# Kernel tuning notes

Measured on AMD Instinct MI355X. Metric: run time of the kernel, lower is better.

The kernel has to match this reference:

```python
import jax, jax.numpy as jnp
import numpy as np


def _conv(x, w, pad):
    # NCHW conv, stride 1
    return jax.lax.conv_general_dilated(
        x, w, window_strides=(1, 1), padding=pad,
        dimension_numbers=("NCHW", "OIHW", "NCHW"))


def _deform_conv(x, off_w, off_b, w, b, kh, kw, ph, pw):
    """DCNv2-style modulated deformable conv, stride 1, zero padding."""
    B, C, H, W = x.shape
    K = kh * kw
    om = _conv(x, off_w, ((ph, ph), (pw, pw))) + off_b[None, :, None, None]  # [B,3K,H,W]
    dy, dx, m = om[:, :K], om[:, K:2 * K], om[:, 2 * K:]
    mask = jax.nn.sigmoid(m)  # [B,K,H,W]
    ky = (jnp.repeat(jnp.arange(kh), kw) - ph).astype(x.dtype)  # [K]
    kx = (jnp.tile(jnp.arange(kw), kh) - pw).astype(x.dtype)    # [K]
    hh = jnp.arange(H, dtype=x.dtype)[None, None, :, None]
    ww = jnp.arange(W, dtype=x.dtype)[None, None, None, :]
    py = dy + ky[None, :, None, None] + hh  # [B,K,H,W] sampling y
    px = dx + kx[None, :, None, None] + ww  # [B,K,H,W] sampling x
    y0 = jnp.floor(py)
    x0 = jnp.floor(px)
    ty = py - y0
    tx = px - x0
    y0i = y0.astype(jnp.int32)
    x0i = x0.astype(jnp.int32)
    bidx = jnp.arange(B)[:, None, None, None]

    def gather(yi, xi):
        valid = (yi >= 0) & (yi < H) & (xi >= 0) & (xi < W)
        yc = jnp.clip(yi, 0, H - 1)
        xc = jnp.clip(xi, 0, W - 1)
        v = x[bidx, :, yc, xc]  # [B,K,H,W,C]
        return v * valid[..., None].astype(x.dtype)

    val = (gather(y0i, x0i) * ((1 - ty) * (1 - tx))[..., None]
           + gather(y0i, x0i + 1) * ((1 - ty) * tx)[..., None]
           + gather(y0i + 1, x0i) * (ty * (1 - tx))[..., None]
           + gather(y0i + 1, x0i + 1) * (ty * tx)[..., None])
    val = val * mask[..., None]  # modulation
    out = jnp.einsum('bkhwc,ock->bohw', val, w.reshape(w.shape[0], C, K))
    return out + b[None, :, None, None]


def _preprocess(x, w1, b1, w2, b2):
    h = _conv(x, w1, ((0, 0), (0, 0))) + b1[None, :, None, None]
    return _conv(h, w2, ((0, 0), (0, 0))) + b2[None, :, None, None]


def setup_inputs() -> dict:
    key = jax.random.key(0)
    ks = jax.random.split(key, 12)
    B, C, H, W = 4, 64, 256, 256
    k = 3
    s = 0.05
    inp = {
        "a_low": jax.random.normal(ks[0], (B, C, H, W), jnp.float32),
        "a_high": jax.random.normal(ks[1], (B, C, H, W), jnp.float32),
        # preprocess: Conv 64->32 (1x1), Conv 32->64 (1x1)
        "pre_w1": jax.random.normal(ks[2], (C // 2, C, 1, 1), jnp.float32) * s,
        "pre_b1": jnp.zeros((C // 2,), jnp.float32),
        "pre_w2": jax.random.normal(ks[3], (C, C // 2, 1, 1), jnp.float32) * s,
        "pre_b2": jnp.zeros((C,), jnp.float32),
        # column DCN (3x1 kernel): offset/mask conv -> 3*K channels, K=3
        "offc_w": jax.random.normal(ks[4], (3 * k, C, k, 1), jnp.float32) * 0.01,
        "offc_b": jnp.zeros((3 * k,), jnp.float32),
        "wc": jax.random.normal(ks[5], (C, C, k, 1), jnp.float32) * s,
        "bc": jnp.zeros((C,), jnp.float32),
        # row DCN (1x3 kernel)
        "offr_w": jax.random.normal(ks[6], (3 * k, C, 1, k), jnp.float32) * 0.01,
        "offr_b": jnp.zeros((3 * k,), jnp.float32),
        "wr": jax.random.normal(ks[7], (C, C, 1, k), jnp.float32) * s,
        "br": jnp.zeros((C,), jnp.float32),
    }
    return inp


def reference(a_low, a_high, pre_w1, pre_b1, pre_w2, pre_b2,
              offc_w, offc_b, wc, bc, offr_w, offr_b, wr, br):
    a_low = _preprocess(a_low, pre_w1, pre_b1, pre_w2, pre_b2)
    a_high = _preprocess(a_high, pre_w1, pre_b1, pre_w2, pre_b2)
    # column DCN: kernel (3,1), padding (1,0)
    a_low_c = _deform_conv(a_low, offc_w, offc_b, wc, bc, 3, 1, 1, 0)
    a_colum = a_low + jax.nn.sigmoid(a_low_c) * a_high
    # row DCN: kernel (1,3), padding (0,1)
    a_low_r = _deform_conv(a_low, offr_w, offr_b, wr, br, 1, 3, 0, 1)
    a_row = a_low + jax.nn.sigmoid(a_low_r) * a_high
    return a_row + a_colum
```

## Files before the change

kernel.cpp:

```cpp
#include <hip/hip_runtime.h>
#include <hip/hip_fp16.h>
#include <cmath>

namespace {
constexpr int Bn = 4, Cn = 64, Hn = 256, Wn = 256;
constexpr int HWn = Hn * Wn;
constexpr size_t OFF_PRE_LOW  = 0;
constexpr size_t OFF_PRE_HIGH = 33554432;
constexpr size_t OFF_OM_COL   = 67108864;
constexpr size_t OFF_OM_ROW   = 76546048;
constexpr size_t OFF_WOF16    = 85999616;
constexpr size_t OFF_WPACK    = 86013440;
constexpr size_t OFF_WPRE     = 86062592;
constexpr size_t OFF_BEFF     = 86070784;

constexpr int L_WIN  = 0;
constexpr int L_MOFF = 25920;
constexpr int L_MW   = 27456;
constexpr int L_CRD  = 28992;
constexpr int L_MSK  = 29760;
constexpr int L_ZL   = 30528;
constexpr int L_TOT  = 30672;
}

typedef _Float16 f16x8 __attribute__((ext_vector_type(8)));
typedef float f32x4 __attribute__((ext_vector_type(4)));

__device__ __forceinline__ float sigm(float x) { return 1.f / (1.f + __expf(-x)); }
__device__ __forceinline__ __half2 bc2(unsigned u) { return __builtin_bit_cast(__half2, u); }
__device__ __forceinline__ unsigned u32of(__half2 h) { return __builtin_bit_cast(unsigned, h); }

__global__ void k_repack(const float* __restrict__ pw1, const float* __restrict__ pw2,
                         const float* __restrict__ b1,  const float* __restrict__ b2,
                         const float* __restrict__ owc, const float* __restrict__ owr,
                         const float* __restrict__ wc,  const float* __restrict__ wr,
                         char* __restrict__ ws8)
{
    unsigned* Wo2  = (unsigned*)(ws8 + OFF_WOF16);
    __half*   Wp   = (__half*)(ws8 + OFF_WPACK);
    __half*   Wpre = (__half*)(ws8 + OFF_WPRE);
    float*    Beff = (float*)(ws8 + OFF_BEFF);
    int t = blockIdx.x * 256 + threadIdx.x;
    int stride = gridDim.x * 256;
    for (int i = t; i < 3456; i += stride) {
        int ck = i / 18, d = i - ck * 18;
        float v = (d < 9) ? owc[d * 192 + ck] : owr[(d - 9) * 192 + ck];
        Wo2[i] = u32of(__float2half2_rn(v));
    }
    for (int i = t; i < 24576; i += stride) {
        int m = i >= 12288;
        int rem = i - m * 12288;
        int e = rem & 7, l = (rem >> 3) & 63, os = (rem >> 9) & 3, s = rem >> 11;
        int kk = 32 * s + (l >> 4) * 8 + e;
        int o = os * 16 + (l & 15);
        int c = kk & 63, tap = kk >> 6;
        const float* src = m ? wr : wc;
        Wp[i] = __float2half(src[o * 192 + c * 3 + tap]);
    }
    for (int i = t; i < 4096; i += stride) {
        int e = i & 7, l = (i >> 3) & 63, os = (i >> 9) & 3, s = i >> 11;
        int o = os * 16 + (l & 15);
        int c = 32 * s + (l >> 4) * 8 + e;
        float a = 0.f;
        for (int j = 0; j < 32; j++) a += pw2[o * 32 + j] * pw1[j * 64 + c];
        Wpre[i] = __float2half(a);
    }
    for (int i = t; i < 64; i += stride) {
        float a = b2[i];
        for (int j = 0; j < 32; j++) a += pw2[i * 32 + j] * b1[j];
        Beff[i] = a;
    }
}

__global__ __launch_bounds__(256) void k_pre(const float* __restrict__ alow,
                                             const float* __restrict__ ahigh,
                                             char* __restrict__ ws8,
                                             __half* __restrict__ anchw)
{
    __shared__ __align__(16) char XSb[32768];
    int bid = blockIdx.x;
    int tensor = bid >> 10;
    int r = bid & 1023;
    int b = r >> 8, h = r & 255;
    const float* __restrict__ x = (tensor ? ahigh : alow)
                                  + (size_t)b * Cn * HWn + (size_t)h * Wn;
    int tid = threadIdx.x;

#pragma unroll
    for (int it = 0; it < 4; it++) {
        int job = tid + it * 256;
        int c4 = job >> 6, pxg = job & 63;
        int c0 = c4 * 4;
        float4 f0 = *reinterpret_cast<const float4*>(x + (size_t)(c0 + 0) * HWn + pxg * 4);
        float4 f1 = *reinterpret_cast<const float4*>(x + (size_t)(c0 + 1) * HWn + pxg * 4);
        float4 f2 = *reinterpret_cast<const float4*>(x + (size_t)(c0 + 2) * HWn + pxg * 4);
        float4 f3 = *reinterpret_cast<const float4*>(x + (size_t)(c0 + 3) * HWn + pxg * 4);
        const float* p0 = reinterpret_cast<const float*>(&f0);
        const float* p1 = reinterpret_cast<const float*>(&f1);
        const float* p2 = reinterpret_cast<const float*>(&f2);
        const float* p3 = reinterpret_cast<const float*>(&f3);
        int u = c4 >> 1, hf = c4 & 1;
#pragma unroll
        for (int i = 0; i < 4; i++) {
            int px = pxg * 4 + i;
            uint2 v;
            v.x = u32of(__float22half2_rn({p0[i], p1[i]}));
            v.y = u32of(__float22half2_rn({p2[i], p3[i]}));
            *reinterpret_cast<uint2*>(XSb + px * 128 + ((u ^ (px & 7)) * 16) + hf * 8) = v;
        }
    }
    __syncthreads();

    int wv = tid >> 6, lane = tid & 63;
    int kq = lane >> 4, n = lane & 15;
    const f16x8* __restrict__ Wf = (const f16x8*)(ws8 + OFF_WPRE);
    const float* __restrict__ beff = (const float*)(ws8 + OFF_BEFF);
    f16x8 af[8];
#pragma unroll
    for (int i = 0; i < 8; i++) af[i] = Wf[i * 64 + lane];
    f32x4 zero = {0.f, 0.f, 0.f, 0.f};
    f32x4 acc[16];
#pragma unroll
    for (int i = 0; i < 16; i++) acc[i] = zero;
#pragma unroll
    for (int s = 0; s < 2; s++) {
#pragma unroll
        for (int pt = 0; pt < 4; pt++) {
            int px = wv * 64 + pt * 16 + n;
            int u = (4 * s + kq) ^ (px & 7);
            f16x8 bf = *reinterpret_cast<const f16x8*>(XSb + px * 128 + u * 16);
#pragma unroll
            for (int os = 0; os < 4; os++)
                acc[os * 4 + pt] = __builtin_amdgcn_mfma_f32_16x16x32_f16(
                    af[s * 4 + os], bf, acc[os * 4 + pt], 0, 0, 0);
        }
    }
#pragma unroll
    for (int os = 0; os < 4; os++) {
        float4 bq = *reinterpret_cast<const float4*>(beff + os * 16 + kq * 4);
        const float* bqp = reinterpret_cast<const float*>(&bq);
#pragma unroll
        for (int pt = 0; pt < 4; pt++)
#pragma unroll
            for (int rg = 0; rg < 4; rg++) acc[os * 4 + pt][rg] += bqp[rg];
    }

    {
        __half* __restrict__ outp = (__half*)(ws8 + (tensor ? OFF_PRE_HIGH : OFF_PRE_LOW))
                                    + (size_t)r * 16384;
#pragma unroll
        for (int os = 0; os < 4; os++)
#pragma unroll
            for (int pt = 0; pt < 4; pt++) {
                int px = wv * 64 + pt * 16 + n;
                uint2 v;
                v.x = u32of(__float22half2_rn({acc[os * 4 + pt][0], acc[os * 4 + pt][1]}));
                v.y = u32of(__float22half2_rn({acc[os * 4 + pt][2], acc[os * 4 + pt][3]}));
                *reinterpret_cast<uint2*>(outp + (size_t)px * 64 + os * 16 + kq * 4) = v;
            }
    }
    if (tensor == 0) {
        __half* __restrict__ np = anchw + (size_t)b * Cn * HWn + (size_t)h * Wn;
#pragma unroll
        for (int os = 0; os < 4; os++)
#pragma unroll
            for (int rg = 0; rg < 4; rg++) {
                int o = os * 16 + kq * 4 + rg;
#pragma unroll
                for (int pt = 0; pt < 4; pt++) {
                    int px = wv * 64 + pt * 16 + n;
                    np[(size_t)o * HWn + px] = __float2half(acc[os * 4 + pt][rg]);
                }
            }
    }
}

__global__ __launch_bounds__(256) void k_om2(const __half* __restrict__ Anc,
                                             const float* __restrict__ ocb,
                                             const float* __restrict__ orb,
                                             char* __restrict__ ws8)
{
    const unsigned* __restrict__ Wo2 = (const unsigned*)(ws8 + OFF_WOF16);
    int blk = blockIdx.x;
    int h = blk & 255, b = blk >> 8;
    int tid = threadIdx.x;
    int q2 = tid & 127, md = tid >> 7;
    int w0 = q2 * 2;
    const __half* __restrict__ base = Anc + ((size_t)b * Cn) * HWn + (size_t)h * Wn + w0;

    const bool topOK = (h > 0), botOK = (h < Hn - 1);
    const bool lOK = (w0 > 0), rOK = (w0 + 2 < Wn);
    const int offT = topOK ? -Wn : 0;
    const int offB = botOK ? Wn : 0;
    const int offL = lOK ? -1 : 0;
    const int offR = rOK ? 2 : 1;

    const __half2 z = __float2half2_rn(0.f);
    const __half hz = __float2half(0.f);
    __half2 a[9];
#pragma unroll
    for (int d = 0; d < 9; d++) a[d] = z;

    if (md == 0) {
        for (int c = 0; c < 64; c++) {
            const __half* pc = base + (size_t)c * HWn;
            unsigned qm = *reinterpret_cast<const unsigned*>(pc + offT);
            unsigned q0 = *reinterpret_cast<const unsigned*>(pc);
            unsigned qp = *reinterpret_cast<const unsigned*>(pc + offB);
            __half2 m0 = topOK ? bc2(qm) : z;
            __half2 c0 = bc2(q0);
            __half2 p0 = botOK ? bc2(qp) : z;
            const unsigned* wb = Wo2 + c * 54;
#pragma unroll
            for (int d = 0; d < 9; d++) {
                __half2 u0 = bc2(wb[d]), u1 = bc2(wb[18 + d]), u2 = bc2(wb[36 + d]);
                a[d] = __hfma2(u0, m0, __hfma2(u1, c0, __hfma2(u2, p0, a[d])));
            }
        }
        float* __restrict__ omc = (float*)(ws8 + OFF_OM_COL);
        size_t ob = ((size_t)b * 9) * HWn + (size_t)h * Wn + w0;
#pragma unroll
        for (int d = 0; d < 9; d++) {
            float bcd = ocb[d];
            float2 vc = { __low2float(a[d]) + bcd, __high2float(a[d]) + bcd };
            *reinterpret_cast<float2*>(omc + ob + (size_t)d * HWn) = vc;
        }
    } else {
        for (int c = 0; c < 64; c++) {
            const __half* pc = base + (size_t)c * HWn;
            unsigned q0 = *reinterpret_cast<const unsigned*>(pc);
            __half L = lOK ? pc[offL] : hz;
            __half R = rOK ? pc[offR] : hz;
            __half2 c0 = bc2(q0);
            __half2 X = __halves2half2(L, __low2half(c0));
            __half2 Z = __halves2half2(__high2half(c0), R);
            const unsigned* wb = Wo2 + c * 54;
#pragma unroll
            for (int d = 0; d < 9; d++) {
                __half2 v0 = bc2(wb[9 + d]), v1 = bc2(wb[27 + d]), v2 = bc2(wb[45 + d]);
                a[d] = __hfma2(v0, X, __hfma2(v1, c0, __hfma2(v2, Z, a[d])));
            }
        }
        float* __restrict__ omr = (float*)(ws8 + OFF_OM_ROW);
        size_t ob = ((size_t)b * 9) * HWn + (size_t)h * Wn + w0;
#pragma unroll
        for (int d = 0; d < 9; d++) {
            float brd = orb[d];
            float2 vr = { __low2float(a[d]) + brd, __high2float(a[d]) + brd };
            *reinterpret_cast<float2*>(omr + ob + (size_t)d * HWn) = vr;
        }
    }
}

__global__ __launch_bounds__(256, 5) void k_dfuse(const float* __restrict__ bc,
                                                  const float* __restrict__ br,
                                                  float* __restrict__ out,
                                                  char* __restrict__ ws8)
{
    __shared__ __align__(16) char smem8[L_TOT];

    const __half* __restrict__ A16 = (const __half*)(ws8 + OFF_PRE_LOW);

    int bid = blockIdx.x;
    int blk = (bid & 7) * 1024 + (bid >> 3);
    int wt = blk & 7, bh = blk >> 3, h = bh & 255, b = bh >> 8;
    int w0 = wt * 32;
    int tid = threadIdx.x;
    int pbase = b * HWn;

    {
        int ylo = h - 2, xlo = w0 - 2;
#pragma unroll
        for (int i = 0; i < 6; i++) {
            int idx = tid + i * 256;
            if (idx < 1440) {
                int pixw = idx >> 3, ch = idx & 7;
                int r = pixw / 36;
                int xi = pixw - r * 36;
                int y = min(max(ylo + r, 0), Hn - 1);
                int x = min(max(xlo + xi, 0), Wn - 1);
                size_t src = ((size_t)pbase + y * Wn + x) * 64 + ch * 8;
                *reinterpret_cast<uint4*>(smem8 + L_WIN + pixw * 144 + ch * 16) =
                    *reinterpret_cast<const uint4*>(A16 + src);
            }
        }
    }
    if (tid >= 192 && tid < 201) {
        uint4 z4 = {0u, 0u, 0u, 0u};
        *reinterpret_cast<uint4*>(smem8 + L_ZL + (tid - 192) * 16) = z4;
    }

    if (tid < 192) {
        int m = tid >= 96 ? 1 : 0;
        int jj = tid - m * 96;
        int p = jj & 31, tap = jj >> 5;
        int w = w0 + p;
        const float* __restrict__ om = (const float*)(ws8 + (m ? OFF_OM_ROW : OFF_OM_COL));
        size_t ob = ((size_t)b * 9 * Hn + h) * Wn + w;
        float dy = om[ob + (size_t)tap * HWn];
        float dx = om[ob + (size_t)(3 + tap) * HWn];
        float mm = om[ob + (size_t)(6 + tap) * HWn];
        float mask = sigm(mm);
        float py = dy + (float)h + (m ? 0.f : (float)(tap - 1));
        float px = dx + (float)w + (m ? (float)(tap - 1) : 0.f);
        float fy = floorf(py), fx = floorf(px);
        float ty = py - fy, tx = px - fx;
        int y0 = (int)fy, x0 = (int)fx;
        int y1 = y0 + 1, x1 = x0 + 1;
        float vy0 = ((unsigned)y0 < (unsigned)Hn) ? 1.f : 0.f;
        float vy1 = ((unsigned)y1 < (unsigned)Hn) ? 1.f : 0.f;
        float vx0 = ((unsigned)x0 < (unsigned)Wn) ? 1.f : 0.f;
        float vx1 = ((unsigned)x1 < (unsigned)Wn) ? 1.f : 0.f;
        int y0c = min(max(y0, 0), Hn - 1), y1c = min(max(y1, 0), Hn - 1);
        int x0c = min(max(x0, 0), Wn - 1), x1c = min(max(x1, 0), Wn - 1);
        float ry = 1.f - ty, rx = 1.f - tx;
        float w00 = ry * rx * mask * vy0 * vx0;
        float w01 = ry * tx * mask * vy0 * vx1;
        float w10 = ty * rx * mask * vy1 * vx0;
        float w11 = ty * tx * mask * vy1 * vx1;
        int yw0 = y0c - (h - 2), yw1 = y1c - (h - 2);
        int xw0 = x0c - (w0 - 2), xw1 = x1c - (w0 - 2);
        bool i00 = ((unsigned)yw0 < 5u) && ((unsigned)xw0 < 36u);
        bool i01 = ((unsigned)yw0 < 5u) && ((unsigned)xw1 < 36u);
        bool i10 = ((unsigned)yw1 < 5u) && ((unsigned)xw0 < 36u);
        bool i11 = ((unsigned)yw1 < 5u) && ((unsigned)xw1 < 36u);
        ushort4 offs;
        offs.x = i00 ? (ushort)((yw0 * 36 + xw0) * 144) : (ushort)L_ZL;
        offs.y = i01 ? (ushort)((yw0 * 36 + xw1) * 144) : (ushort)L_ZL;
        offs.z = i10 ? (ushort)((yw1 * 36 + xw0) * 144) : (ushort)L_ZL;
        offs.w = i11 ? (ushort)((yw1 * 36 + xw1) * 144) : (ushort)L_ZL;
        *reinterpret_cast<ushort4*>(smem8 + L_MOFF + tid * 8) = offs;
        __half* mw = reinterpret_cast<__half*>(smem8 + L_MW + tid * 8);
        mw[0] = __float2half(w00); mw[1] = __float2half(w01);
        mw[2] = __float2half(w10); mw[3] = __float2half(w11);
        uchar4 cr = { (unsigned char)y0c, (unsigned char)x0c,
                      (unsigned char)y1c, (unsigned char)x1c };
        *reinterpret_cast<uchar4*>(smem8 + L_CRD + tid * 4) = cr;
        unsigned msk = (i00 ? 0u : 1u) | (i01 ? 0u : 2u) | (i10 ? 0u : 4u) | (i11 ? 0u : 8u);
        *reinterpret_cast<unsigned*>(smem8 + L_MSK + tid * 4) = msk;
    }
    __syncthreads();

    int wv = tid >> 6, lane = tid & 63;
    int m = wv >> 1, pg = wv & 1;
    int n = lane & 15, kq = lane >> 4;
    int p = pg * 16 + n;
    const f16x8* __restrict__ Wf = (const f16x8*)(ws8 + OFF_WPACK + (size_t)m * 24576);

    f32x4 zero = {0.f, 0.f, 0.f, 0.f};
    f32x4 acc[4] = {zero, zero, zero, zero};
    ushort4 offs = {0, 0, 0, 0};
    __half2 wh0 = {}, wh1 = {}, wh2 = {}, wh3 = {};
    unsigned msk = 0;
    uchar4 cr = {0, 0, 0, 0};
#pragma unroll
    for (int s = 0; s < 6; s++) {
        if ((s & 1) == 0) {
            int idx = m * 96 + (s >> 1) * 32 + p;
            offs = *reinterpret_cast<const ushort4*>(smem8 + L_MOFF + idx * 8);
            uint2 wr_ = *reinterpret_cast<const uint2*>(smem8 + L_MW + idx * 8);
            __half2 wa = bc2(wr_.x), wb = bc2(wr_.y);
            wh0 = __half2half2(__low2half(wa));
            wh1 = __half2half2(__high2half(wa));
            wh2 = __half2half2(__low2half(wb));
            wh3 = __half2half2(__high2half(wb));
            msk = *reinterpret_cast<const unsigned*>(smem8 + L_MSK + idx * 4);
            cr = *reinterpret_cast<const uchar4*>(smem8 + L_CRD + idx * 4);
        }
        int co = ((s & 1) << 6) + kq * 16;
        uint4 u0 = *reinterpret_cast<const uint4*>(smem8 + (int)offs.x + co);
        uint4 u1 = *reinterpret_cast<const uint4*>(smem8 + (int)offs.y + co);
        uint4 u2 = *reinterpret_cast<const uint4*>(smem8 + (int)offs.z + co);
        uint4 u3 = *reinterpret_cast<const uint4*>(smem8 + (int)offs.w + co);
        __half2 a0 = __hmul2(bc2(u0.x), wh0);
        __half2 a1 = __hmul2(bc2(u0.y), wh0);
        __half2 a2 = __hmul2(bc2(u0.z), wh0);
        __half2 a3 = __hmul2(bc2(u0.w), wh0);
        a0 = __hfma2(bc2(u1.x), wh1, a0); a1 = __hfma2(bc2(u1.y), wh1, a1);
        a2 = __hfma2(bc2(u1.z), wh1, a2); a3 = __hfma2(bc2(u1.w), wh1, a3);
        a0 = __hfma2(bc2(u2.x), wh2, a0); a1 = __hfma2(bc2(u2.y), wh2, a1);
        a2 = __hfma2(bc2(u2.z), wh2, a2); a3 = __hfma2(bc2(u2.w), wh2, a3);
        a0 = __hfma2(bc2(u3.x), wh3, a0); a1 = __hfma2(bc2(u3.y), wh3, a1);
        a2 = __hfma2(bc2(u3.z), wh3, a2); a3 = __hfma2(bc2(u3.w), wh3, a3);
        if (__any(msk != 0)) {
            int cog = ((s & 1) << 5) + kq * 8;
            if (msk & 1u) {
                int gx = (pbase + (int)cr.x * Wn + (int)cr.y) * 64;
                uint4 u = *reinterpret_cast<const uint4*>(A16 + gx + cog);
                a0 = __hfma2(bc2(u.x), wh0, a0); a1 = __hfma2(bc2(u.y), wh0, a1);
                a2 = __hfma2(bc2(u.z), wh0, a2); a3 = __hfma2(bc2(u.w), wh0, a3); }
            if (msk & 2u) {
                int gx = (pbase + (int)cr.x * Wn + (int)cr.w) * 64;
                uint4 u = *reinterpret_cast<const uint4*>(A16 + gx + cog);
                a0 = __hfma2(bc2(u.x), wh1, a0); a1 = __hfma2(bc2(u.y), wh1, a1);
                a2 = __hfma2(bc2(u.z), wh1, a2); a3 = __hfma2(bc2(u.w), wh1, a3); }
            if (msk & 4u) {
                int gx = (pbase + (int)cr.z * Wn + (int)cr.y) * 64;
                uint4 u = *reinterpret_cast<const uint4*>(A16 + gx + cog);
                a0 = __hfma2(bc2(u.x), wh2, a0); a1 = __hfma2(bc2(u.y), wh2, a1);
                a2 = __hfma2(bc2(u.z), wh2, a2); a3 = __hfma2(bc2(u.w), wh2, a3); }
            if (msk & 8u) {
                int gx = (pbase + (int)cr.z * Wn + (int)cr.w) * 64;
                uint4 u = *reinterpret_cast<const uint4*>(A16 + gx + cog);
                a0 = __hfma2(bc2(u.x), wh3, a0); a1 = __hfma2(bc2(u.y), wh3, a1);
                a2 = __hfma2(bc2(u.z), wh3, a2); a3 = __hfma2(bc2(u.w), wh3, a3); }
        }
        uint4 hb = { u32of(a0), u32of(a1), u32of(a2), u32of(a3) };
        f16x8 bf = __builtin_bit_cast(f16x8, hb);
#pragma unroll
        for (int os = 0; os < 4; os++)
            acc[os] = __builtin_amdgcn_mfma_f32_16x16x32_f16(Wf[(s * 4 + os) * 64 + lane], bf, acc[os], 0, 0, 0);
    }

    const float* __restrict__ bias = m ? br : bc;
    float sg[4][4];
#pragma unroll
    for (int os = 0; os < 4; os++) {
        float4 bq = *reinterpret_cast<const float4*>(bias + os * 16 + kq * 4);
        const float* bqp = reinterpret_cast<const float*>(&bq);
#pragma unroll
        for (int rg = 0; rg < 4; rg++) sg[os][rg] = sigm(acc[os][rg] + bqp[rg]);
    }
    __syncthreads();
    float* EXf = reinterpret_cast<float*>(smem8);
#pragma unroll
    for (int os = 0; os < 4; os++)
#pragma unroll
        for (int rg = 0; rg < 4; rg++)
            EXf[m * 2176 + (os * 16 + kq * 4 + rg) * 34 + p] = sg[os][rg];
    __syncthreads();

    int p2 = tid & 31, og = tid >> 5;
    int o0 = og * 8;
    size_t pix = ((size_t)b * Hn + h) * Wn + (w0 + p2);
    uint4 ua = *reinterpret_cast<const uint4*>(A16 + pix * 64 + o0);
    const __half* ap = reinterpret_cast<const __half*>(&ua);
    const __half* __restrict__ Ah16 = (const __half*)(ws8 + OFF_PRE_HIGH);
    uint4 uh = *reinterpret_cast<const uint4*>(Ah16 + pix * 64 + o0);
    const __half* hp = reinterpret_cast<const __half*>(&uh);
    size_t chbase = ((size_t)b * 64 + o0) * HWn + (size_t)h * Wn + (w0 + p2);
#pragma unroll
    for (int j = 0; j < 8; j++) {
        float sc = EXf[(o0 + j) * 34 + p2];
        float sr = EXf[2176 + (o0 + j) * 34 + p2];
        float av = __half2float(ap[j]);
        float hv = __half2float(hp[j]);
        out[chbase + (size_t)j * HWn] = 2.f * av + (sc + sr) * hv;
    }
}

extern "C" void kernel_launch(void* const* d_in, const int* in_sizes, int n_in,
                              void* d_out, int out_size, void* d_ws, size_t ws_size,
                              hipStream_t stream)
{
    const float* a_low  = (const float*)d_in[0];
    const float* a_high = (const float*)d_in[1];
    const float* pre_w1 = (const float*)d_in[2];
    const float* pre_b1 = (const float*)d_in[3];
    const float* pre_w2 = (const float*)d_in[4];
    const float* pre_b2 = (const float*)d_in[5];
    const float* offc_w = (const float*)d_in[6];
    const float* offc_b = (const float*)d_in[7];
    const float* wc     = (const float*)d_in[8];
    const float* bc     = (const float*)d_in[9];
    const float* offr_w = (const float*)d_in[10];
    const float* offr_b = (const float*)d_in[11];
    const float* wr     = (const float*)d_in[12];
    const float* br     = (const float*)d_in[13];
    float* out = (float*)d_out;
    char* ws8  = (char*)d_ws;

    hipLaunchKernelGGL(k_repack, dim3(128), dim3(256), 0, stream,
                       pre_w1, pre_w2, pre_b1, pre_b2, offc_w, offr_w, wc, wr, ws8);
    hipLaunchKernelGGL(k_pre, dim3(2048), dim3(256), 0, stream,
                       a_low, a_high, ws8, (__half*)d_out);
    hipLaunchKernelGGL(k_om2, dim3(1024), dim3(256), 0, stream,
                       (const __half*)d_out, offc_b, offr_b, ws8);
    hipLaunchKernelGGL(k_dfuse, dim3(8192), dim3(256), 0, stream,
                       bc, br, out, ws8);
}
```

Baseline: 157.9 us.

## Store offset maps in fp16, add block-uniform in-window fast path, vectorize epilogue LDS

The offset/mask conv output is now written and read as fp16 instead of fp32, halving that intermediate traffic. A __syncthreads_or over per-sample out-of-window flags lets blocks where every sample falls inside the shared-memory window skip the global-fallback branch and its mask/coordinate loads. The sampling offsets and weights for all three taps are preloaded into registers up front. The sigmoid exchange buffer is transposed to pixel-major so writes and reads use float4 LDS accesses. The change costs offset precision (fp16 rounding of dy/dx before floor) and adds register pressure from the hoisted tap data.

```diff
diff --git a/kernel.cpp b/kernel.cpp
--- a/kernel.cpp
+++ b/kernel.cpp
@@ -8,7 +8,7 @@
 constexpr size_t OFF_PRE_LOW  = 0;
 constexpr size_t OFF_PRE_HIGH = 33554432;
 constexpr size_t OFF_OM_COL   = 67108864;
-constexpr size_t OFF_OM_ROW   = 76546048;
+constexpr size_t OFF_OM_ROW   = 71827456;
 constexpr size_t OFF_WOF16    = 85999616;
 constexpr size_t OFF_WPACK    = 86013440;
 constexpr size_t OFF_WPRE     = 86062592;
@@ -217,13 +217,12 @@
                 a[d] = __hfma2(u0, m0, __hfma2(u1, c0, __hfma2(u2, p0, a[d])));
             }
         }
-        float* __restrict__ omc = (float*)(ws8 + OFF_OM_COL);
+        __half* __restrict__ omc = (__half*)(ws8 + OFF_OM_COL);
         size_t ob = ((size_t)b * 9) * HWn + (size_t)h * Wn + w0;
 #pragma unroll
         for (int d = 0; d < 9; d++) {
-            float bcd = ocb[d];
-            float2 vc = { __low2float(a[d]) + bcd, __high2float(a[d]) + bcd };
-            *reinterpret_cast<float2*>(omc + ob + (size_t)d * HWn) = vc;
+            __half2 v = __hadd2(a[d], __float2half2_rn(ocb[d]));
+            *reinterpret_cast<unsigned*>(omc + ob + (size_t)d * HWn) = u32of(v);
         }
     } else {
         for (int c = 0; c < 64; c++) {
@@ -241,13 +240,12 @@
                 a[d] = __hfma2(v0, X, __hfma2(v1, c0, __hfma2(v2, Z, a[d])));
             }
         }
-        float* __restrict__ omr = (float*)(ws8 + OFF_OM_ROW);
+        __half* __restrict__ omr = (__half*)(ws8 + OFF_OM_ROW);
         size_t ob = ((size_t)b * 9) * HWn + (size_t)h * Wn + w0;
 #pragma unroll
         for (int d = 0; d < 9; d++) {
-            float brd = orb[d];
-            float2 vr = { __low2float(a[d]) + brd, __high2float(a[d]) + brd };
-            *reinterpret_cast<float2*>(omr + ob + (size_t)d * HWn) = vr;
+            __half2 v = __hadd2(a[d], __float2half2_rn(orb[d]));
+            *reinterpret_cast<unsigned*>(omr + ob + (size_t)d * HWn) = u32of(v);
         }
     }
 }
@@ -290,16 +288,17 @@
         *reinterpret_cast<uint4*>(smem8 + L_ZL + (tid - 192) * 16) = z4;
     }
 
+    int myMsk = 0;
     if (tid < 192) {
         int m = tid >= 96 ? 1 : 0;
         int jj = tid - m * 96;
         int p = jj & 31, tap = jj >> 5;
         int w = w0 + p;
-        const float* __restrict__ om = (const float*)(ws8 + (m ? OFF_OM_ROW : OFF_OM_COL));
+        const __half* __restrict__ om = (const __half*)(ws8 + (m ? OFF_OM_ROW : OFF_OM_COL));
         size_t ob = ((size_t)b * 9 * Hn + h) * Wn + w;
-        float dy = om[ob + (size_t)tap * HWn];
-        float dx = om[ob + (size_t)(3 + tap) * HWn];
-        float mm = om[ob + (size_t)(6 + tap) * HWn];
+        float dy = __half2float(om[ob + (size_t)tap * HWn]);
+        float dx = __half2float(om[ob + (size_t)(3 + tap) * HWn]);
+        float mm = __half2float(om[ob + (size_t)(6 + tap) * HWn]);
         float mask = sigm(mm);
         float py = dy + (float)h + (m ? 0.f : (float)(tap - 1));
         float px = dx + (float)w + (m ? (float)(tap - 1) : 0.f);
@@ -336,10 +335,10 @@
         uchar4 cr = { (unsigned char)y0c, (unsigned char)x0c,
                       (unsigned char)y1c, (unsigned char)x1c };
         *reinterpret_cast<uchar4*>(smem8 + L_CRD + tid * 4) = cr;
-        unsigned msk = (i00 ? 0u : 1u) | (i01 ? 0u : 2u) | (i10 ? 0u : 4u) | (i11 ? 0u : 8u);
-        *reinterpret_cast<unsigned*>(smem8 + L_MSK + tid * 4) = msk;
-    }
-    __syncthreads();
+        myMsk = (i00 ? 0 : 1) | (i01 ? 0 : 2) | (i10 ? 0 : 4) | (i11 ? 0 : 8);
+        *reinterpret_cast<unsigned*>(smem8 + L_MSK + tid * 4) = (unsigned)myMsk;
+    }
+    int anyOOW = __syncthreads_or(myMsk);
 
     int wv = tid >> 6, lane = tid & 63;
     int m = wv >> 1, pg = wv & 1;
@@ -347,70 +346,93 @@
     int p = pg * 16 + n;
     const f16x8* __restrict__ Wf = (const f16x8*)(ws8 + OFF_WPACK + (size_t)m * 24576);
 
+    ushort4 offs[3];
+    __half2 wh[3][4];
+#pragma unroll
+    for (int t3 = 0; t3 < 3; t3++) {
+        int idx = m * 96 + t3 * 32 + p;
+        offs[t3] = *reinterpret_cast<const ushort4*>(smem8 + L_MOFF + idx * 8);
+        uint2 wr_ = *reinterpret_cast<const uint2*>(smem8 + L_MW + idx * 8);
+        __half2 wa = bc2(wr_.x), wb = bc2(wr_.y);
+        wh[t3][0] = __half2half2(__low2half(wa));
+        wh[t3][1] = __half2half2(__high2half(wa));
+        wh[t3][2] = __half2half2(__low2half(wb));
+        wh[t3][3] = __half2half2(__high2half(wb));
+    }
+
     f32x4 zero = {0.f, 0.f, 0.f, 0.f};
     f32x4 acc[4] = {zero, zero, zero, zero};
-    ushort4 offs = {0, 0, 0, 0};
-    __half2 wh0 = {}, wh1 = {}, wh2 = {}, wh3 = {};
-    unsigned msk = 0;
-    uchar4 cr = {0, 0, 0, 0};
-#pragma unroll
-    for (int s = 0; s < 6; s++) {
-        if ((s & 1) == 0) {
-            int idx = m * 96 + (s >> 1) * 32 + p;
-            offs = *reinterpret_cast<const ushort4*>(smem8 + L_MOFF + idx * 8);
-            uint2 wr_ = *reinterpret_cast<const uint2*>(smem8 + L_MW + idx * 8);
-            __half2 wa = bc2(wr_.x), wb = bc2(wr_.y);
-            wh0 = __half2half2(__low2half(wa));
-            wh1 = __half2half2(__high2half(wa));
-            wh2 = __half2half2(__low2half(wb));
-            wh3 = __half2half2(__high2half(wb));
-            msk = *reinterpret_cast<const unsigned*>(smem8 + L_MSK + idx * 4);
-            cr = *reinterpret_cast<const uchar4*>(smem8 + L_CRD + idx * 4);
-        }
-        int co = ((s & 1) << 6) + kq * 16;
-        uint4 u0 = *reinterpret_cast<const uint4*>(smem8 + (int)offs.x + co);
-        uint4 u1 = *reinterpret_cast<const uint4*>(smem8 + (int)offs.y + co);
-        uint4 u2 = *reinterpret_cast<const uint4*>(smem8 + (int)offs.z + co);
-        uint4 u3 = *reinterpret_cast<const uint4*>(smem8 + (int)offs.w + co);
-        __half2 a0 = __hmul2(bc2(u0.x), wh0);
-        __half2 a1 = __hmul2(bc2(u0.y), wh0);
-        __half2 a2 = __hmul2(bc2(u0.z), wh0);
-        __half2 a3 = __hmul2(bc2(u0.w), wh0);
-        a0 = __hfma2(bc2(u1.x), wh1, a0); a1 = __hfma2(bc2(u1.y), wh1, a1);
-        a2 = __hfma2(bc2(u1.z), wh1, a2); a3 = __hfma2(bc2(u1.w), wh1, a3);
-        a0 = __hfma2(bc2(u2.x), wh2, a0); a1 = __hfma2(bc2(u2.y), wh2, a1);
-        a2 = __hfma2(bc2(u2.z), wh2, a2); a3 = __hfma2(bc2(u2.w), wh2, a3);
-        a0 = __hfma2(bc2(u3.x), wh3, a0); a1 = __hfma2(bc2(u3.y), wh3, a1);
-        a2 = __hfma2(bc2(u3.z), wh3, a2); a3 = __hfma2(bc2(u3.w), wh3, a3);
-        if (__any(msk != 0)) {
-            int cog = ((s & 1) << 5) + kq * 8;
-            if (msk & 1u) {
-                int gx = (pbase + (int)cr.x * Wn + (int)cr.y) * 64;
-                uint4 u = *reinterpret_cast<const uint4*>(A16 + gx + cog);
-                a0 = __hfma2(bc2(u.x), wh0, a0); a1 = __hfma2(bc2(u.y), wh0, a1);
-                a2 = __hfma2(bc2(u.z), wh0, a2); a3 = __hfma2(bc2(u.w), wh0, a3); }
-            if (msk & 2u) {
-                int gx = (pbase + (int)cr.x * Wn + (int)cr.w) * 64;
-                uint4 u = *reinterpret_cast<const uint4*>(A16 + gx + cog);
-                a0 = __hfma2(bc2(u.x), wh1, a0); a1 = __hfma2(bc2(u.y), wh1, a1);
-                a2 = __hfma2(bc2(u.z), wh1, a2); a3 = __hfma2(bc2(u.w), wh1, a3); }
-            if (msk & 4u) {
-                int gx = (pbase + (int)cr.z * Wn + (int)cr.y) * 64;
-                uint4 u = *reinterpret_cast<const uint4*>(A16 + gx + cog);
-                a0 = __hfma2(bc2(u.x), wh2, a0); a1 = __hfma2(bc2(u.y), wh2, a1);
-                a2 = __hfma2(bc2(u.z), wh2, a2); a3 = __hfma2(bc2(u.w), wh2, a3); }
-            if (msk & 8u) {
-                int gx = (pbase + (int)cr.z * Wn + (int)cr.w) * 64;
-                uint4 u = *reinterpret_cast<const uint4*>(A16 + gx + cog);
-                a0 = __hfma2(bc2(u.x), wh3, a0); a1 = __hfma2(bc2(u.y), wh3, a1);
-                a2 = __hfma2(bc2(u.z), wh3, a2); a3 = __hfma2(bc2(u.w), wh3, a3); }
-        }
-        uint4 hb = { u32of(a0), u32of(a1), u32of(a2), u32of(a3) };
-        f16x8 bf = __builtin_bit_cast(f16x8, hb);
-#pragma unroll
-        for (int os = 0; os < 4; os++)
-            acc[os] = __builtin_amdgcn_mfma_f32_16x16x32_f16(Wf[(s * 4 + os) * 64 + lane], bf, acc[os], 0, 0, 0);
-    }
+
+#define GBLEND(T, CO, A0, A1, A2, A3)                                            \
+    {                                                                            \
+        uint4 u0 = *reinterpret_cast<const uint4*>(smem8 + (int)offs[T].x + (CO)); \
+        uint4 u1 = *reinterpret_cast<const uint4*>(smem8 + (int)offs[T].y + (CO)); \
+        uint4 u2 = *reinterpret_cast<const uint4*>(smem8 + (int)offs[T].z + (CO)); \
+        uint4 u3 = *reinterpret_cast<const uint4*>(smem8 + (int)offs[T].w + (CO)); \
+        A0 = __hmul2(bc2(u0.x), wh[T][0]); A1 = __hmul2(bc2(u0.y), wh[T][0]);    \
+        A2 = __hmul2(bc2(u0.z), wh[T][0]); A3 = __hmul2(bc2(u0.w), wh[T][0]);    \
+        A0 = __hfma2(bc2(u1.x), wh[T][1], A0); A1 = __hfma2(bc2(u1.y), wh[T][1], A1); \
+        A2 = __hfma2(bc2(u1.z), wh[T][1], A2); A3 = __hfma2(bc2(u1.w), wh[T][1], A3); \
+        A0 = __hfma2(bc2(u2.x), wh[T][2], A0); A1 = __hfma2(bc2(u2.y), wh[T][2], A1); \
+        A2 = __hfma2(bc2(u2.z), wh[T][2], A2); A3 = __hfma2(bc2(u2.w), wh[T][2], A3); \
+        A0 = __hfma2(bc2(u3.x), wh[T][3], A0); A1 = __hfma2(bc2(u3.y), wh[T][3], A1); \
+        A2 = __hfma2(bc2(u3.z), wh[T][3], A2); A3 = __hfma2(bc2(u3.w), wh[T][3], A3); \
+    }
+
+    if (!anyOOW) {
+#pragma unroll
+        for (int s = 0; s < 6; s++) {
+            int t3 = s >> 1;
+            int co = ((s & 1) << 6) + kq * 16;
+            __half2 a0, a1, a2, a3;
+            GBLEND(t3, co, a0, a1, a2, a3);
+            uint4 hb = { u32of(a0), u32of(a1), u32of(a2), u32of(a3) };
+            f16x8 bf = __builtin_bit_cast(f16x8, hb);
+#pragma unroll
+            for (int os = 0; os < 4; os++)
+                acc[os] = __builtin_amdgcn_mfma_f32_16x16x32_f16(Wf[(s * 4 + os) * 64 + lane], bf, acc[os], 0, 0, 0);
+        }
+    } else {
+#pragma unroll
+        for (int s = 0; s < 6; s++) {
+            int t3 = s >> 1;
+            int co = ((s & 1) << 6) + kq * 16;
+            __half2 a0, a1, a2, a3;
+            GBLEND(t3, co, a0, a1, a2, a3);
+            int idx = m * 96 + t3 * 32 + p;
+            unsigned msk = *reinterpret_cast<const unsigned*>(smem8 + L_MSK + idx * 4);
+            uchar4 cr = *reinterpret_cast<const uchar4*>(smem8 + L_CRD + idx * 4);
+            if (__any(msk != 0)) {
+                int cog = ((s & 1) << 5) + kq * 8;
+                if (msk & 1u) {
+                    int gx = (pbase + (int)cr.x * Wn + (int)cr.y) * 64;
+                    uint4 u = *reinterpret_cast<const uint4*>(A16 + gx + cog);
+                    a0 = __hfma2(bc2(u.x), wh[t3][0], a0); a1 = __hfma2(bc2(u.y), wh[t3][0], a1);
+                    a2 = __hfma2(bc2(u.z), wh[t3][0], a2); a3 = __hfma2(bc2(u.w), wh[t3][0], a3); }
+                if (msk & 2u) {
+                    int gx = (pbase + (int)cr.x * Wn + (int)cr.w) * 64;
+                    uint4 u = *reinterpret_cast<const uint4*>(A16 + gx + cog);
+                    a0 = __hfma2(bc2(u.x), wh[t3][1], a0); a1 = __hfma2(bc2(u.y), wh[t3][1], a1);
+                    a2 = __hfma2(bc2(u.z), wh[t3][1], a2); a3 = __hfma2(bc2(u.w), wh[t3][1], a3); }
+                if (msk & 4u) {
+                    int gx = (pbase + (int)cr.z * Wn + (int)cr.y) * 64;
+                    uint4 u = *reinterpret_cast<const uint4*>(A16 + gx + cog);
+                    a0 = __hfma2(bc2(u.x), wh[t3][2], a0); a1 = __hfma2(bc2(u.y), wh[t3][2], a1);
+                    a2 = __hfma2(bc2(u.z), wh[t3][2], a2); a3 = __hfma2(bc2(u.w), wh[t3][2], a3); }
+                if (msk & 8u) {
+                    int gx = (pbase + (int)cr.z * Wn + (int)cr.w) * 64;
+                    uint4 u = *reinterpret_cast<const uint4*>(A16 + gx + cog);
+                    a0 = __hfma2(bc2(u.x), wh[t3][3], a0); a1 = __hfma2(bc2(u.y), wh[t3][3], a1);
+                    a2 = __hfma2(bc2(u.z), wh[t3][3], a2); a3 = __hfma2(bc2(u.w), wh[t3][3], a3); }
+            }
+            uint4 hb = { u32of(a0), u32of(a1), u32of(a2), u32of(a3) };
+            f16x8 bf = __builtin_bit_cast(f16x8, hb);
+#pragma unroll
+            for (int os = 0; os < 4; os++)
+                acc[os] = __builtin_amdgcn_mfma_f32_16x16x32_f16(Wf[(s * 4 + os) * 64 + lane], bf, acc[os], 0, 0, 0);
+        }
+    }
+#undef GBLEND
 
     const float* __restrict__ bias = m ? br : bc;
     float sg[4][4];
@@ -424,10 +446,10 @@
     __syncthreads();
     float* EXf = reinterpret_cast<float*>(smem8);
 #pragma unroll
-    for (int os = 0; os < 4; os++)
-#pragma unroll
-        for (int rg = 0; rg < 4; rg++)
-            EXf[m * 2176 + (os * 16 + kq * 4 + rg) * 34 + p] = sg[os][rg];
+    for (int os = 0; os < 4; os++) {
+        float4 v = { sg[os][0], sg[os][1], sg[os][2], sg[os][3] };
+        *reinterpret_cast<float4*>(&EXf[m * 2176 + p * 68 + os * 16 + kq * 4]) = v;
+    }
     __syncthreads();
 
     int p2 = tid & 31, og = tid >> 5;
@@ -438,14 +460,26 @@
     const __half* __restrict__ Ah16 = (const __half*)(ws8 + OFF_PRE_HIGH);
     uint4 uh = *reinterpret_cast<const uint4*>(Ah16 + pix * 64 + o0);
     const __half* hp = reinterpret_cast<const __half*>(&uh);
+    float4 ec0 = *reinterpret_cast<const float4*>(&EXf[p2 * 68 + o0]);
+    float4 ec1 = *reinterpret_cast<const float4*>(&EXf[p2 * 68 + o0 + 4]);
+    float4 er0 = *reinterpret_cast<const float4*>(&EXf[2176 + p2 * 68 + o0]);
+    float4 er1 = *reinterpret_cast<const float4*>(&EXf[2176 + p2 * 68 + o0 + 4]);
+    const float* ecp = reinterpret_cast<const float*>(&ec0);
+    const float* erp = reinterpret_cast<const float*>(&er0);
+    const float* ecq = reinterpret_cast<const float*>(&ec1);
+    const float* erq = reinterpret_cast<const float*>(&er1);
     size_t chbase = ((size_t)b * 64 + o0) * HWn + (size_t)h * Wn + (w0 + p2);
 #pragma unroll
-    for (int j = 0; j < 8; j++) {
-        float sc = EXf[(o0 + j) * 34 + p2];
-        float sr = EXf[2176 + (o0 + j) * 34 + p2];
+    for (int j = 0; j < 4; j++) {
         float av = __half2float(ap[j]);
         float hv = __half2float(hp[j]);
-        out[chbase + (size_t)j * HWn] = 2.f * av + (sc + sr) * hv;
+        out[chbase + (size_t)j * HWn] = 2.f * av + (ecp[j] + erp[j]) * hv;
+    }
+#pragma unroll
+    for (int j = 0; j < 4; j++) {
+        float av = __half2float(ap[4 + j]);
+        float hv = __half2float(hp[4 + j]);
+        out[chbase + (size_t)(4 + j) * HWn] = 2.f * av + (ecq[j] + erq[j]) * hv;
     }
 }
 
```

After: 153.6 us. 2.7% less time.
